# Kernel optimization log

Hardware: AMD Instinct MI355X
Metric: run time of the kernel (lower is better)

Reference implementation:

```python
import jax, jax.numpy as jnp
import numpy as np

B, T, CNN, HW = 512, 256, 512, 7
V, H = 37, 8  # vocab_size, hidden_size


def setup_inputs() -> dict:
    key = jax.random.key(0)
    ks = jax.random.split(key, 10)
    s = 0.1
    return {
        "features": jax.random.normal(ks[0], (B, CNN, HW, HW), jnp.float32),
        "captions": jax.random.normal(ks[1], (B, T, V), jnp.float32),
        "W_in": jax.random.normal(ks[2], (V, CNN), jnp.float32) * s,
        "b_in": jax.random.normal(ks[3], (V,), jnp.float32) * s,
        "W_ih": jax.random.normal(ks[4], (4 * H, V), jnp.float32) * s,
        "W_hh": jax.random.normal(ks[5], (4 * H, H), jnp.float32) * s,
        "b_ih": jax.random.normal(ks[6], (4 * H,), jnp.float32) * s,
        "b_hh": jax.random.normal(ks[7], (4 * H,), jnp.float32) * s,
        "W_out": jax.random.normal(ks[8], (V, H), jnp.float32) * s,
        "b_out": jax.random.normal(ks[9], (V,), jnp.float32) * s,
    }


def reference(features, captions, W_in, b_in, W_ih, W_hh, b_ih, b_hh, W_out, b_out):
    # AdaptiveAvgPool2d(1) + flatten + fc_in -> [B, V]
    feat = features.mean(axis=(2, 3)) @ W_in.T + b_in
    # input at t=0 is feat, at t>0 is captions[:, t-1]; build [T, B, V] sequence
    xs = jnp.concatenate([feat[None], jnp.swapaxes(captions, 0, 1)[:-1]], axis=0)

    def step(carry, x):
        h, c = carry
        gates = x @ W_ih.T + b_ih + h @ W_hh.T + b_hh  # [B, 4H]
        i, f, g, o = jnp.split(gates, 4, axis=1)  # PyTorch LSTMCell gate order
        i = jax.nn.sigmoid(i)
        f = jax.nn.sigmoid(f)
        g = jnp.tanh(g)
        o = jax.nn.sigmoid(o)
        c = f * c + i * g
        h = o * jnp.tanh(c)
        out = jax.nn.softmax(h @ W_out.T + b_out, axis=1)  # [B, V]
        return (h, c), out

    h0 = jnp.zeros((feat.shape[0], W_hh.shape[1]), feat.dtype)
    c0 = jnp.zeros_like(h0)
    _, outs = jax.lax.scan(step, (h0, c0), xs)  # outs: [T, B, V]
    return jnp.swapaxes(outs, 0, 1)  # [B, T, V]
```

## Files before the change

### kernel.cpp

```cpp
#include <hip/hip_runtime.h>
#include <math.h>

#define BB   512
#define TT   256
#define CNNC 512
#define VV   37
#define HH   8
#define G4   32
#define CH   32
#define CW   (CH * 128)

#define L2E 1.4426950408889634f

typedef float f4_t __attribute__((ext_vector_type(4)));

__device__ __forceinline__ void async_copy16(const float* g, float* l) {
    __builtin_amdgcn_global_load_lds(
        (__attribute__((address_space(1))) void*)g,
        (__attribute__((address_space(3))) void*)l, 16, 0, 0);
}

template <int CTRL>
__device__ __forceinline__ float dpp_f(float x) {
    int r = __builtin_amdgcn_update_dpp(0, __float_as_int(x), CTRL, 0xF, 0xF, true);
    return __int_as_float(r);
}

__device__ __forceinline__ float rcp_f(float x) { return __builtin_amdgcn_rcpf(x); }
__device__ __forceinline__ float exp2_f(float x) { return __builtin_amdgcn_exp2f(x); }

__global__ __launch_bounds__(256) void k_feat(const float* __restrict__ features,
                                              const float* __restrict__ W_in,
                                              const float* __restrict__ b_in,
                                              float* __restrict__ featp) {
    __shared__ __align__(16) float raw[128 * 49];
    __shared__ float pooled[128];
    const int b = blockIdx.x, qt = blockIdx.y, tid = threadIdx.x;
    const f4_t* src =
        (const f4_t*)(features + (size_t)b * CNNC * 49 + qt * (128 * 49));
    f4_t* dst = (f4_t*)raw;
    for (int i = tid; i < 128 * 49 / 4; i += 256)
        dst[i] = __builtin_nontemporal_load(&src[i]);
    __syncthreads();
    if (tid < 128) {
        const float* p = raw + tid * 49;
        float s = 0.f;
        #pragma unroll
        for (int i = 0; i < 49; ++i) s += p[i];
        pooled[tid] = s;
    }
    __syncthreads();
    const int v = tid >> 2, pp = tid & 3;
    if (v < VV) {
        const float* w = W_in + v * CNNC + qt * 128 + pp * 32;
        const float* q = pooled + pp * 32;
        float s = 0.f;
        #pragma unroll
        for (int i = 0; i < 32; ++i) s += q[i] * w[i];
        s += __shfl_xor(s, 1);
        s += __shfl_xor(s, 2);
        if (pp == 0)
            featp[(qt * BB + b) * VV + v] =
                s * (1.f / 49.f) + (qt == 0 ? b_in[v] : 0.f);
    }
}

#define CAPS 1188
#define SOS  132
__global__ __launch_bounds__(256) void k_xproj(const float* __restrict__ captions,
                                               const float* __restrict__ W_ih,
                                               const float* __restrict__ b_ih,
                                               const float* __restrict__ b_hh,
                                               const float* __restrict__ featp,
                                               float* __restrict__ xproj) {
    __shared__ float W[G4 * VV];
    __shared__ float bias[G4];
    __shared__ float cap[4 * CAPS];
    __shared__ __align__(16) float so[32 * SOS];
    const int bg = blockIdx.x, tile = blockIdx.y;
    const int tid = threadIdx.x;
    for (int i = tid; i < G4 * VV; i += 256) W[i] = W_ih[i];
    if (tid < G4) bias[tid] = b_ih[tid] + b_hh[tid];

    const int t0 = tile * 32;
    const int start = (tile == 0) ? 0 : t0 - 1;
    for (int i = tid; i < 4 * 1184; i += 256) {
        const int s2 = i / 1184;
        const int off = i - s2 * 1184;
        cap[s2 * CAPS + off] = __builtin_nontemporal_load(
            &captions[((size_t)(bg * 4 + s2) * TT + start) * VV + off]);
    }
    __syncthreads();

    const int tl = tid >> 3;
    const int s  = (tid >> 1) & 3;
    const int r  = tid & 1;
    const int t  = t0 + tl;
    const int b  = bg * 4 + s;

    float xr[VV];
    if (tile == 0 && tl == 0) {
        #pragma unroll
        for (int v = 0; v < VV; ++v)
            xr[v] = featp[b * VV + v] + featp[(BB + b) * VV + v] +
                    featp[(2 * BB + b) * VV + v] + featp[(3 * BB + b) * VV + v];
    } else {
        const int lr = (tile == 0) ? tl - 1 : tl;
        const float* x = &cap[s * CAPS + lr * VV];
        #pragma unroll
        for (int v = 0; v < VV; ++v) xr[v] = x[v];
    }

    const int g0 = r * 16;
    float acc[16];
    #pragma unroll
    for (int g = 0; g < 16; ++g) acc[g] = bias[g0 + g];
    #pragma unroll
    for (int v = 0; v < VV; ++v) {
        const float xv = xr[v];
        #pragma unroll
        for (int g = 0; g < 16; ++g) acc[g] += xv * W[(g0 + g) * VV + v];
    }
    #pragma unroll
    for (int g = 0; g < 16; ++g) {
        const int gg = g0 + g;
        const float sc = (gg >= 16 && gg < 24) ? (-2.f * L2E) : (-L2E);
        so[tl * SOS + gg * 4 + s] = acc[g] * sc;
    }
    __syncthreads();

    float* chunk = xproj + ((size_t)bg * TT + t0) * 128;
    for (int i = tid; i < 1024; i += 256) {
        const int t2 = i >> 5, rest = i & 31;
        f4_t val = *(const f4_t*)&so[t2 * SOS + rest * 4];
        *(f4_t*)&chunk[t2 * 128 + rest * 4] = val;
    }
}

__global__ __launch_bounds__(64) void k_lstm(const float* __restrict__ W_hh,
                                             const float* __restrict__ xproj,
                                             float* __restrict__ hbuf) {
    __shared__ __align__(16) float buf[3 * CW + 128];
    const int lane = threadIdx.x;
    const int s4 = lane >> 4;
    const int q  = lane & 15;
    const int j  = q >> 1;
    const int r  = q & 1;

    const int rowA = r * 8 + j;
    const int rowB = 16 + r * 8 + j;
    const float scA = -L2E;
    const float scB = r ? -L2E : (-2.f * L2E);
    float wA[HH], wB[HH];
    #pragma unroll
    for (int m = 0; m < HH; ++m) {
        wA[m] = scA * W_hh[rowA * HH + (j ^ m)];
        wB[m] = scB * W_hh[rowB * HH + (j ^ m)];
    }

    const int bg = blockIdx.x;
    const float* xp = xproj + (size_t)bg * (TT * 128);
    float* hb = hbuf + ((size_t)(bg * 4 + s4) * TT) * HH + j;
    const int roff = rowA * 4 + s4;

    #pragma unroll
    for (int it = 0; it < 16; ++it)
        async_copy16(xp + (it * 64 + lane) * 4, &buf[it * 256]);
    #pragma unroll
    for (int it = 0; it < 16; ++it)
        async_copy16(xp + CW + (it * 64 + lane) * 4, &buf[CW + it * 256]);

    float h = 0.f, c = 0.f;
    for (int ck = 0; ck < TT / CH; ++ck) {
        if (ck == 0)      asm volatile("s_waitcnt vmcnt(16)" ::: "memory");
        else if (ck == 7) asm volatile("s_waitcnt vmcnt(32)" ::: "memory");
        else              asm volatile("s_waitcnt vmcnt(48)" ::: "memory");

        const float* base = &buf[(ck % 3) * CW] + roff;
        float hsv[CH];
        float pA = base[0], pB = base[64];
        #pragma unroll
        for (int tl = 0; tl < CH; ++tl) {
            const float nA = base[(tl + 1) * 128];
            const float nB = base[(tl + 1) * 128 + 64];

            const float ha0 = h;
            const float ha1 = dpp_f<0x4E>(h);
            const float ha3 = dpp_f<0x141>(h);
            const float ha2 = dpp_f<0x4E>(ha3);
            const float ha7 = dpp_f<0x140>(h);
            const float ha4 = dpp_f<0x141>(ha7);
            const float ha5 = dpp_f<0x4E>(ha4);
            const float ha6 = dpp_f<0x1B>(ha7);

            float a0 = fmaf(wA[0], ha0, pA);
            a0 = fmaf(wA[1], ha1, a0);
            a0 = fmaf(wA[2], ha2, a0);
            a0 = fmaf(wA[3], ha3, a0);
            float a1 = wA[4] * ha4;
            a1 = fmaf(wA[5], ha5, a1);
            a1 = fmaf(wA[6], ha6, a1);
            a1 = fmaf(wA[7], ha7, a1);
            const float npA = a0 + a1;
            float b0 = fmaf(wB[0], ha0, pB);
            b0 = fmaf(wB[1], ha1, b0);
            b0 = fmaf(wB[2], ha2, b0);
            b0 = fmaf(wB[3], ha3, b0);
            float b1 = wB[4] * ha4;
            b1 = fmaf(wB[5], ha5, b1);
            b1 = fmaf(wB[6], ha6, b1);
            b1 = fmaf(wB[7], ha7, b1);
            const float npB = b0 + b1;

            const float eA = rcp_f(1.f + exp2_f(npA));
            const float uB = rcp_f(1.f + exp2_f(npB));
            const float gg = fmaf(2.f, uB, -1.f);

            const float myU = r ? eA : eA * gg;
            const float otU = dpp_f<0xB1>(myU);
            const float fg  = r ? myU : otU;
            const float igg = r ? otU : myU;
            const float ogx = dpp_f<0xB1>(uB);
            const float og  = r ? uB : ogx;

            c = fmaf(fg, c, igg);
            const float th =
                fmaf(2.f, rcp_f(1.f + exp2_f(c * (-2.f * L2E))), -1.f);
            h = og * th;
            hsv[tl] = h;
            pA = nA; pB = nB;
        }
        if (r == 0) {
            #pragma unroll
            for (int i = 0; i < CH; ++i) hb[(ck * CH + i) * HH] = hsv[i];
        }
        if (ck + 2 < TT / CH) {
            const float* src = xp + (size_t)(ck + 2) * CW;
            float* db = &buf[((ck + 2) % 3) * CW];
            #pragma unroll
            for (int it = 0; it < 16; ++it)
                async_copy16(src + (it * 64 + lane) * 4, &db[it * 256]);
        }
    }
}

__global__ __launch_bounds__(128) void k_out(const float* __restrict__ hbuf,
                                             const float* __restrict__ W_out,
                                             const float* __restrict__ b_out,
                                             float* __restrict__ out) {
    __shared__ float W[VV * HH];
    __shared__ float bo[VV];
    __shared__ __align__(16) float stage[128 * VV];
    const int b = blockIdx.x, half = blockIdx.y, tid = threadIdx.x;
    for (int i = tid; i < VV * HH; i += 128) W[i] = W_out[i];
    if (tid < VV) bo[tid] = b_out[tid];
    __syncthreads();

    const int t = half * 128 + tid;
    const f4_t* hp = (const f4_t*)(hbuf + ((size_t)b * TT + t) * HH);
    const f4_t h0 = hp[0], h1 = hp[1];
    const float hr[HH] = {h0.x, h0.y, h0.z, h0.w, h1.x, h1.y, h1.z, h1.w};

    float z[VV];
    float m = -1e30f;
    #pragma unroll
    for (int v = 0; v < VV; ++v) {
        float sv = bo[v];
        #pragma unroll
        for (int k = 0; k < HH; ++k) sv += hr[k] * W[v * HH + k];
        z[v] = sv;
        m = fmaxf(m, sv);
    }
    float sum = 0.f;
    #pragma unroll
    for (int v = 0; v < VV; ++v) {
        z[v] = exp2_f((z[v] - m) * L2E);
        sum += z[v];
    }
    const float rs = rcp_f(sum);
    #pragma unroll
    for (int v = 0; v < VV; ++v) stage[tid * VV + v] = z[v] * rs;
    __syncthreads();

    f4_t* ob = (f4_t*)(out + ((size_t)b * TT + half * 128) * VV);
    const f4_t* sg = (const f4_t*)stage;
    for (int i = tid; i < 128 * VV / 4; i += 128)
        __builtin_nontemporal_store(sg[i], &ob[i]);
}

extern "C" void kernel_launch(void* const* d_in, const int* in_sizes, int n_in,
                              void* d_out, int out_size, void* d_ws, size_t ws_size,
                              hipStream_t stream) {
    const float* features = (const float*)d_in[0];
    const float* captions = (const float*)d_in[1];
    const float* W_in     = (const float*)d_in[2];
    const float* b_in     = (const float*)d_in[3];
    const float* W_ih     = (const float*)d_in[4];
    const float* W_hh     = (const float*)d_in[5];
    const float* b_ih     = (const float*)d_in[6];
    const float* b_hh     = (const float*)d_in[7];
    const float* W_out    = (const float*)d_in[8];
    const float* b_out    = (const float*)d_in[9];
    float* out = (float*)d_out;

    float* ws    = (float*)d_ws;
    float* featp = ws;
    float* xproj = ws + 81920;
    float* hbuf  = ws + 81920 + 4194304;

    k_feat <<<dim3(BB, 4),  256, 0, stream>>>(features, W_in, b_in, featp);
    k_xproj<<<dim3(128, 8), 256, 0, stream>>>(captions, W_ih, b_ih, b_hh, featp, xproj);
    k_lstm <<<128,           64, 0, stream>>>(W_hh, xproj, hbuf);
    k_out  <<<dim3(BB, 2),  128, 0, stream>>>(hbuf, W_out, b_out, out);
}
```

Baseline: 195.7 us.

## Fuse output projection and softmax into LSTM kernel with producer/consumer waves

Merges the output softmax kernel into the recurrent kernel. One wave runs the recurrence and writes each chunk of hidden states into a double-buffered shared-memory area, while two extra waves compute the output projection and softmax for the previous chunk, synchronised by a barrier per chunk. This removes the hbuf round trip through global memory and one kernel launch, and overlaps output work with the serial recurrence. It also folds the gate scaling constants into the tanh-argument computation. The risks are that the per-chunk barriers stall the critical recurrence wave, and that outputs are now written as uncoalesced per-thread scalar stores instead of staged vector nontemporal stores.

```diff
diff --git a/kernel.cpp b/kernel.cpp
--- a/kernel.cpp
+++ b/kernel.cpp
@@ -137,155 +137,163 @@
     }
 }
 
-__global__ __launch_bounds__(64) void k_lstm(const float* __restrict__ W_hh,
-                                             const float* __restrict__ xproj,
-                                             float* __restrict__ hbuf) {
+__global__ __launch_bounds__(192) void k_lstm(const float* __restrict__ W_hh,
+                                              const float* __restrict__ xproj,
+                                              const float* __restrict__ W_out,
+                                              const float* __restrict__ b_out,
+                                              float* __restrict__ out) {
     __shared__ __align__(16) float buf[3 * CW + 128];
-    const int lane = threadIdx.x;
+    __shared__ __align__(16) float hst[2 * 4 * CH * HH];
+    __shared__ __align__(16) float Wo[VV * HH];
+    __shared__ float bo[VV];
+
+    const int tid  = threadIdx.x;
+    const int wv   = tid >> 6;
+    const int lane = tid & 63;
+    const int bg   = blockIdx.x;
+    const float* xp = xproj + (size_t)bg * (TT * 128);
+
+    if (wv == 0) {
+        #pragma unroll
+        for (int it = 0; it < 16; ++it)
+            async_copy16(xp + (it * 64 + lane) * 4, &buf[it * 256]);
+        #pragma unroll
+        for (int it = 0; it < 16; ++it)
+            async_copy16(xp + CW + (it * 64 + lane) * 4, &buf[CW + it * 256]);
+    } else {
+        const int l2 = tid - 64;
+        for (int i = l2; i < VV * HH; i += 128) Wo[i] = W_out[i];
+        if (l2 < VV) bo[l2] = b_out[l2];
+    }
+
     const int s4 = lane >> 4;
     const int q  = lane & 15;
     const int j  = q >> 1;
     const int r  = q & 1;
-
-    const int rowA = r * 8 + j;
-    const int rowB = 16 + r * 8 + j;
-    const float scA = -L2E;
-    const float scB = r ? -L2E : (-2.f * L2E);
     float wA[HH], wB[HH];
-    #pragma unroll
-    for (int m = 0; m < HH; ++m) {
-        wA[m] = scA * W_hh[rowA * HH + (j ^ m)];
-        wB[m] = scB * W_hh[rowB * HH + (j ^ m)];
-    }
-
-    const int bg = blockIdx.x;
-    const float* xp = xproj + (size_t)bg * (TT * 128);
-    float* hb = hbuf + ((size_t)(bg * 4 + s4) * TT) * HH + j;
-    const int roff = rowA * 4 + s4;
-
-    #pragma unroll
-    for (int it = 0; it < 16; ++it)
-        async_copy16(xp + (it * 64 + lane) * 4, &buf[it * 256]);
-    #pragma unroll
-    for (int it = 0; it < 16; ++it)
-        async_copy16(xp + CW + (it * 64 + lane) * 4, &buf[CW + it * 256]);
-
+    int roff = 0;
+    if (wv == 0) {
+        const int rowA = r * 8 + j;
+        const int rowB = 16 + r * 8 + j;
+        const float scA = -L2E;
+        const float scB = r ? -L2E : (-2.f * L2E);
+        #pragma unroll
+        for (int m = 0; m < HH; ++m) {
+            wA[m] = scA * W_hh[rowA * HH + (j ^ m)];
+            wB[m] = scB * W_hh[rowB * HH + (j ^ m)];
+        }
+        roff = rowA * 4 + s4;
+    }
     float h = 0.f, c = 0.f;
-    for (int ck = 0; ck < TT / CH; ++ck) {
-        if (ck == 0)      asm volatile("s_waitcnt vmcnt(16)" ::: "memory");
-        else if (ck == 7) asm volatile("s_waitcnt vmcnt(32)" ::: "memory");
-        else              asm volatile("s_waitcnt vmcnt(48)" ::: "memory");
-
-        const float* base = &buf[(ck % 3) * CW] + roff;
-        float hsv[CH];
-        float pA = base[0], pB = base[64];
-        #pragma unroll
-        for (int tl = 0; tl < CH; ++tl) {
-            const float nA = base[(tl + 1) * 128];
-            const float nB = base[(tl + 1) * 128 + 64];
-
-            const float ha0 = h;
-            const float ha1 = dpp_f<0x4E>(h);
-            const float ha3 = dpp_f<0x141>(h);
-            const float ha2 = dpp_f<0x4E>(ha3);
-            const float ha7 = dpp_f<0x140>(h);
-            const float ha4 = dpp_f<0x141>(ha7);
-            const float ha5 = dpp_f<0x4E>(ha4);
-            const float ha6 = dpp_f<0x1B>(ha7);
-
-            float a0 = fmaf(wA[0], ha0, pA);
-            a0 = fmaf(wA[1], ha1, a0);
-            a0 = fmaf(wA[2], ha2, a0);
-            a0 = fmaf(wA[3], ha3, a0);
-            float a1 = wA[4] * ha4;
-            a1 = fmaf(wA[5], ha5, a1);
-            a1 = fmaf(wA[6], ha6, a1);
-            a1 = fmaf(wA[7], ha7, a1);
-            const float npA = a0 + a1;
-            float b0 = fmaf(wB[0], ha0, pB);
-            b0 = fmaf(wB[1], ha1, b0);
-            b0 = fmaf(wB[2], ha2, b0);
-            b0 = fmaf(wB[3], ha3, b0);
-            float b1 = wB[4] * ha4;
-            b1 = fmaf(wB[5], ha5, b1);
-            b1 = fmaf(wB[6], ha6, b1);
-            b1 = fmaf(wB[7], ha7, b1);
-            const float npB = b0 + b1;
-
-            const float eA = rcp_f(1.f + exp2_f(npA));
-            const float uB = rcp_f(1.f + exp2_f(npB));
-            const float gg = fmaf(2.f, uB, -1.f);
-
-            const float myU = r ? eA : eA * gg;
-            const float otU = dpp_f<0xB1>(myU);
-            const float fg  = r ? myU : otU;
-            const float igg = r ? otU : myU;
-            const float ogx = dpp_f<0xB1>(uB);
-            const float og  = r ? uB : ogx;
-
-            c = fmaf(fg, c, igg);
-            const float th =
-                fmaf(2.f, rcp_f(1.f + exp2_f(c * (-2.f * L2E))), -1.f);
-            h = og * th;
-            hsv[tl] = h;
-            pA = nA; pB = nB;
+
+    const int orow = (wv - 1) * 64 + lane;
+    const int os   = orow >> 5;
+    const int otl  = orow & 31;
+
+    for (int it = 0; it < 9; ++it) {
+        if (wv == 0) {
+            if (it < 8) {
+                if (it == 0)      asm volatile("s_waitcnt vmcnt(16)" ::: "memory");
+                else if (it == 7) asm volatile("s_waitcnt vmcnt(32)" ::: "memory");
+                else              asm volatile("s_waitcnt vmcnt(48)" ::: "memory");
+
+                const float* base = &buf[(it % 3) * CW] + roff;
+                float* hsl = &hst[((it & 1) * 4 + s4) * (CH * HH) + j];
+                float pA = base[0], pB = base[64];
+                #pragma unroll
+                for (int tl = 0; tl < CH; ++tl) {
+                    const float nA = base[(tl + 1) * 128];
+                    const float nB = base[(tl + 1) * 128 + 64];
+
+                    const float ha0 = h;
+                    const float ha1 = dpp_f<0x4E>(h);
+                    const float ha3 = dpp_f<0x141>(h);
+                    const float ha2 = dpp_f<0x4E>(ha3);
+                    const float ha7 = dpp_f<0x140>(h);
+                    const float ha4 = dpp_f<0x141>(ha7);
+                    const float ha5 = dpp_f<0x4E>(ha4);
+                    const float ha6 = dpp_f<0x1B>(ha7);
+
+                    float a0 = fmaf(wA[0], ha0, pA);
+                    a0 = fmaf(wA[1], ha1, a0);
+                    a0 = fmaf(wA[2], ha2, a0);
+                    a0 = fmaf(wA[3], ha3, a0);
+                    float a1 = wA[4] * ha4;
+                    a1 = fmaf(wA[5], ha5, a1);
+                    a1 = fmaf(wA[6], ha6, a1);
+                    a1 = fmaf(wA[7], ha7, a1);
+                    const float npA = a0 + a1;
+                    float b0 = fmaf(wB[0], ha0, pB);
+                    b0 = fmaf(wB[1], ha1, b0);
+                    b0 = fmaf(wB[2], ha2, b0);
+                    b0 = fmaf(wB[3], ha3, b0);
+                    float b1 = wB[4] * ha4;
+                    b1 = fmaf(wB[5], ha5, b1);
+                    b1 = fmaf(wB[6], ha6, b1);
+                    b1 = fmaf(wB[7], ha7, b1);
+                    const float npB = b0 + b1;
+
+                    const float eA = rcp_f(1.f + exp2_f(npA));
+                    const float uB = rcp_f(1.f + exp2_f(npB));
+                    const float gg = fmaf(-4.f * L2E, uB, 2.f * L2E);
+
+                    const float myU = r ? eA : eA * gg;
+                    const float otU = dpp_f<0xB1>(myU);
+                    const float fg  = r ? myU : otU;
+                    const float igg = r ? otU : myU;
+                    const float ogx = dpp_f<0xB1>(uB);
+                    const float og  = r ? uB : ogx;
+
+                    c = fmaf(fg, c, igg);
+                    const float th = fmaf(2.f, rcp_f(1.f + exp2_f(c)), -1.f);
+                    h = og * th;
+                    if (r == 0) hsl[tl * HH] = h;
+                    pA = nA; pB = nB;
+                }
+                if (it + 2 < TT / CH) {
+                    const float* src = xp + (size_t)(it + 2) * CW;
+                    float* db = &buf[((it + 2) % 3) * CW];
+                    #pragma unroll
+                    for (int k = 0; k < 16; ++k)
+                        async_copy16(src + (k * 64 + lane) * 4, &db[k * 256]);
+                }
+            }
+        } else if (it >= 1) {
+            const int pk = it - 1;
+            const f4_t* hp =
+                (const f4_t*)&hst[(((pk & 1) * 4 + os) * CH + otl) * HH];
+            const f4_t h0 = hp[0], h1 = hp[1];
+            const f4_t* W4 = (const f4_t*)Wo;
+            float z[VV];
+            float m = -1e30f;
+            #pragma unroll
+            for (int v = 0; v < VV; ++v) {
+                const f4_t w0 = W4[v * 2], w1 = W4[v * 2 + 1];
+                float sv = bo[v];
+                sv = fmaf(h0.x, w0.x, sv); sv = fmaf(h0.y, w0.y, sv);
+                sv = fmaf(h0.z, w0.z, sv); sv = fmaf(h0.w, w0.w, sv);
+                sv = fmaf(h1.x, w1.x, sv); sv = fmaf(h1.y, w1.y, sv);
+                sv = fmaf(h1.z, w1.z, sv); sv = fmaf(h1.w, w1.w, sv);
+                z[v] = sv;
+                m = fmaxf(m, sv);
+            }
+            float sum = 0.f;
+            #pragma unroll
+            for (int v = 0; v < VV; ++v) {
+                z[v] = exp2_f((z[v] - m) * L2E);
+                sum += z[v];
+            }
+            const float rs = rcp_f(sum);
+            const int b = bg * 4 + os;
+            const int t = pk * CH + otl;
+            float* op = out + ((size_t)b * TT + t) * VV;
+            #pragma unroll
+            for (int v = 0; v < VV; ++v) op[v] = z[v] * rs;
         }
-        if (r == 0) {
-            #pragma unroll
-            for (int i = 0; i < CH; ++i) hb[(ck * CH + i) * HH] = hsv[i];
-        }
-        if (ck + 2 < TT / CH) {
-            const float* src = xp + (size_t)(ck + 2) * CW;
-            float* db = &buf[((ck + 2) % 3) * CW];
-            #pragma unroll
-            for (int it = 0; it < 16; ++it)
-                async_copy16(src + (it * 64 + lane) * 4, &db[it * 256]);
-        }
-    }
-}
-
-__global__ __launch_bounds__(128) void k_out(const float* __restrict__ hbuf,
-                                             const float* __restrict__ W_out,
-                                             const float* __restrict__ b_out,
-                                             float* __restrict__ out) {
-    __shared__ float W[VV * HH];
-    __shared__ float bo[VV];
-    __shared__ __align__(16) float stage[128 * VV];
-    const int b = blockIdx.x, half = blockIdx.y, tid = threadIdx.x;
-    for (int i = tid; i < VV * HH; i += 128) W[i] = W_out[i];
-    if (tid < VV) bo[tid] = b_out[tid];
-    __syncthreads();
-
-    const int t = half * 128 + tid;
-    const f4_t* hp = (const f4_t*)(hbuf + ((size_t)b * TT + t) * HH);
-    const f4_t h0 = hp[0], h1 = hp[1];
-    const float hr[HH] = {h0.x, h0.y, h0.z, h0.w, h1.x, h1.y, h1.z, h1.w};
-
-    float z[VV];
-    float m = -1e30f;
-    #pragma unroll
-    for (int v = 0; v < VV; ++v) {
-        float sv = bo[v];
-        #pragma unroll
-        for (int k = 0; k < HH; ++k) sv += hr[k] * W[v * HH + k];
-        z[v] = sv;
-        m = fmaxf(m, sv);
-    }
-    float sum = 0.f;
-    #pragma unroll
-    for (int v = 0; v < VV; ++v) {
-        z[v] = exp2_f((z[v] - m) * L2E);
-        sum += z[v];
-    }
-    const float rs = rcp_f(sum);
-    #pragma unroll
-    for (int v = 0; v < VV; ++v) stage[tid * VV + v] = z[v] * rs;
-    __syncthreads();
-
-    f4_t* ob = (f4_t*)(out + ((size_t)b * TT + half * 128) * VV);
-    const f4_t* sg = (const f4_t*)stage;
-    for (int i = tid; i < 128 * VV / 4; i += 128)
-        __builtin_nontemporal_store(sg[i], &ob[i]);
+        asm volatile("s_waitcnt lgkmcnt(0)" ::: "memory");
+        __builtin_amdgcn_s_barrier();
+        __builtin_amdgcn_sched_barrier(0);
+    }
 }
 
 extern "C" void kernel_launch(void* const* d_in, const int* in_sizes, int n_in,
@@ -306,10 +314,8 @@
     float* ws    = (float*)d_ws;
     float* featp = ws;
     float* xproj = ws + 81920;
-    float* hbuf  = ws + 81920 + 4194304;
 
     k_feat <<<dim3(BB, 4),  256, 0, stream>>>(features, W_in, b_in, featp);
     k_xproj<<<dim3(128, 8), 256, 0, stream>>>(captions, W_ih, b_ih, b_hh, featp, xproj);
-    k_lstm <<<128,           64, 0, stream>>>(W_hh, xproj, hbuf);
-    k_out  <<<dim3(BB, 2),  128, 0, stream>>>(hbuf, W_out, b_out, out);
-}
+    k_lstm <<<128,          192, 0, stream>>>(W_hh, xproj, W_out, b_out, out);
+}
```

Result: no change. 194.3 us (-0.7%).
